# Kernel optimization log

Measured on AMD Instinct MI355X. Metric: run time of the kernel, lower is better.

## Reference

```python
import math
import jax, jax.numpy as jnp
import numpy as np

B, S, D, H = 1, 4096, 1024, 16
HD = D // H


def setup_inputs() -> dict:
    key = jax.random.key(0)
    ks = jax.random.split(key, 11)
    s = 0.02
    inp = {
        "q": jax.random.normal(ks[0], (B, S, D), jnp.float32),
        "k": jax.random.normal(ks[1], (B, S, D), jnp.float32),
        "v": jax.random.normal(ks[2], (B, S, D), jnp.float32),
        # causal boolean mask, broadcastable over [B, H, S, S]
        "mask": jnp.tril(jnp.ones((S, S), jnp.bool_))[None, None],
        "Wq": jax.random.normal(ks[3], (D, D), jnp.float32) * s,
        "bq": jnp.zeros((D,), jnp.float32),
        "Wk": jax.random.normal(ks[4], (D, D), jnp.float32) * s,
        "bk": jnp.zeros((D,), jnp.float32),
        "Wv": jax.random.normal(ks[5], (D, D), jnp.float32) * s,
        "bv": jnp.zeros((D,), jnp.float32),
        "Wo": jax.random.normal(ks[6], (D, D), jnp.float32) * s,
        "bo": jnp.zeros((D,), jnp.float32),
    }
    return inp


def reference(q, k, v, mask, Wq, bq, Wk, bk, Wv, bv, Wo, bo):
    # projections (torch Linear: x @ W.T + b; here W is stored already transposed)
    qp = (q @ Wq + bq).reshape(B, S, H, HD)
    kp = (k @ Wk + bk).reshape(B, S, H, HD)
    vp = (v @ Wv + bv).reshape(B, S, H, HD)
    # scores: [B, H, S, S]
    scores = jnp.einsum("bqhd,bkhd->bhqk", qp, kp) / math.sqrt(HD)
    scores = jnp.where(mask, scores, -jnp.inf)
    attn = jax.nn.softmax(scores, axis=-1)
    # context: [B, H, S, HD] -> [B, S, D]
    ctx = jnp.einsum("bhqk,bkhd->bqhd", attn, vp).reshape(B, S, D)
    return ctx @ Wo + bo
```

## Files before the change

kernel.cpp:

```cpp
#include <hip/hip_runtime.h>
#include <hip/hip_bf16.h>


#define S_LEN 4096
#define D_DIM 1024
#define NHEAD 16
#define HDIM  64

typedef __hip_bfloat16 bf16;
typedef __attribute__((ext_vector_type(8))) short bf16x8v;
typedef __attribute__((ext_vector_type(4))) float f32x4;
typedef __attribute__((ext_vector_type(2))) unsigned int u32x2;

#define MFMA16(a, b, c) __builtin_amdgcn_mfma_f32_16x16x32_bf16((a), (b), (c), 0, 0, 0)

#if __has_builtin(__builtin_amdgcn_exp2f)
#define EXP2F(x) __builtin_amdgcn_exp2f(x)
#else
#define EXP2F(x) exp2f(x)
#endif

#define QSCALE (0.125f * 1.4426950408889634f)

template<int N> struct IC { static constexpr int value = N; };

__device__ __forceinline__ void async_cp16(const void* g, void* l) {
    __builtin_amdgcn_global_load_lds(
        (const __attribute__((address_space(1))) unsigned int*)g,
        (__attribute__((address_space(3))) unsigned int*)l, 16, 0, 0);
}

__device__ __forceinline__ unsigned int cvtpk_bf16(float lo, float hi) {
    unsigned int r;
    asm("v_cvt_pk_bf16_f32 %0, %1, %2" : "=v"(r) : "v"(lo), "v"(hi));
    return r;
}

__global__ __launch_bounds__(256) void cvt_bf16_k(
    const float* __restrict__ x0, const float* __restrict__ x1,
    const float* __restrict__ x2,
    bf16* __restrict__ y0, bf16* __restrict__ y1, bf16* __restrict__ y2)
{
    const float* x = (blockIdx.z == 0) ? x0 : (blockIdx.z == 1) ? x1 : x2;
    bf16*       y = (blockIdx.z == 0) ? y0 : (blockIdx.z == 1) ? y1 : y2;
    const size_t i = ((size_t)blockIdx.x * 256 + threadIdx.x);
    const float4 v = ((const float4*)x)[i];
    union { bf16 h[4]; short4 s; } u;
    u.h[0] = __float2bfloat16(v.x);
    u.h[1] = __float2bfloat16(v.y);
    u.h[2] = __float2bfloat16(v.z);
    u.h[3] = __float2bfloat16(v.w);
    ((short4*)y)[i] = u.s;
}

__global__ __launch_bounds__(256) void transpose_cvt_k(
    const float* __restrict__ W0, const float* __restrict__ W1,
    const float* __restrict__ W2, const float* __restrict__ W3,
    bf16* __restrict__ T0, bf16* __restrict__ T1,
    bf16* __restrict__ T2, bf16* __restrict__ T3)
{
    const float* W = (blockIdx.z == 0) ? W0 : (blockIdx.z == 1) ? W1
                   : (blockIdx.z == 2) ? W2 : W3;
    bf16*       Wt = (blockIdx.z == 0) ? T0 : (blockIdx.z == 1) ? T1
                   : (blockIdx.z == 2) ? T2 : T3;
    __shared__ float t[32][33];
    const int bx = blockIdx.x << 5, by = blockIdx.y << 5;
    const int tx = threadIdx.x & 31, ty = threadIdx.x >> 5;
#pragma unroll
    for (int i = 0; i < 32; i += 8)
        t[ty + i][tx] = W[(size_t)(by + ty + i) * D_DIM + bx + tx];
    __syncthreads();
#pragma unroll
    for (int i = 0; i < 32; i += 8)
        Wt[(size_t)(bx + ty + i) * D_DIM + by + tx] = __float2bfloat16(t[tx][ty + i]);
}

struct GemmJob {
    const bf16* A; const bf16* Wt; const float* bias; void* out;
    int mode; float scale;
};

__global__ __launch_bounds__(256) void gemm_k(GemmJob j0, GemmJob j1, GemmJob j2)
{
    const GemmJob j = (blockIdx.z == 0) ? j0 : (blockIdx.z == 1) ? j1 : j2;
    const int K = D_DIM;

    const int nx  = gridDim.x;
    const int lin = blockIdx.y * nx + blockIdx.x;
    const int per = (nx * gridDim.y) >> 3;
    const int bmn = (lin & 7) * per + (lin >> 3);
    const int bn = (bmn % nx) << 6;
    const int bm = (bmn / nx) << 7;

    const int tid = threadIdx.x;
    const int w = tid >> 6, lane = tid & 63;
    const int col = lane & 15, g = lane >> 4;
    const int wr = (w >> 1) << 6, wc = (w & 1) << 5;

    __shared__ bf16 As[2][128 * 64];
    __shared__ bf16 Bs[2][64 * 64];

    f32x4 acc[4][2];
#pragma unroll
    for (int i = 0; i < 4; ++i)
#pragma unroll
        for (int jj = 0; jj < 2; ++jj) acc[i][jj] = (f32x4){0.f, 0.f, 0.f, 0.f};

    auto stage = [&](int buf, int kb) {
#pragma unroll
        for (int e = 0; e < 4; ++e) {
            const int l2 = (e << 8) + tid;
            const int row = l2 >> 3, kc = l2 & 7;
            async_cp16(j.A + (size_t)(bm + row) * K + kb + (kc << 3), &As[buf][l2 << 3]);
        }
#pragma unroll
        for (int e = 0; e < 2; ++e) {
            const int l2 = (e << 8) + tid;
            const int row = l2 >> 3, kc = l2 & 7;
            async_cp16(j.Wt + (size_t)(bn + row) * K + kb + (kc << 3), &Bs[buf][l2 << 3]);
        }
    };

    stage(0, 0);
    __syncthreads();
    int cur = 0;

    for (int kb = 0; kb < K; kb += 64) {
        if (kb + 64 < K) stage(cur ^ 1, kb + 64);

#pragma unroll
        for (int s = 0; s < 2; ++s) {
            bf16x8v af[4], bfv[2];
#pragma unroll
            for (int i = 0; i < 4; ++i)
                af[i] = *(const bf16x8v*)&As[cur][((wr + (i << 4) + col) << 6) + (s << 5) + (g << 3)];
#pragma unroll
            for (int jj = 0; jj < 2; ++jj)
                bfv[jj] = *(const bf16x8v*)&Bs[cur][((wc + (jj << 4) + col) << 6) + (s << 5) + (g << 3)];
#pragma unroll
            for (int i = 0; i < 4; ++i)
#pragma unroll
                for (int jj = 0; jj < 2; ++jj)
                    acc[i][jj] = MFMA16(af[i], bfv[jj], acc[i][jj]);
        }

        __syncthreads();
        cur ^= 1;
    }

#pragma unroll
    for (int i = 0; i < 4; ++i)
#pragma unroll
    for (int jj = 0; jj < 2; ++jj)
#pragma unroll
    for (int reg = 0; reg < 4; ++reg) {
        const int row = bm + wr + (i << 4) + (g << 2) + reg;
        const int cg  = bn + wc + (jj << 4) + col;
        const float vv = (acc[i][jj][reg] + j.bias[cg]) * j.scale;
        if (j.mode == 0)
            ((bf16*)j.out)[(((size_t)(cg >> 6)) * S_LEN + row) * HDIM + (cg & 63)] =
                __float2bfloat16(vv);
        else if (j.mode == 2)
            ((bf16*)j.out)[((size_t)(cg >> 6) * HDIM + (cg & 63)) * S_LEN + row] =
                __float2bfloat16(vv);
        else
            ((float*)j.out)[(size_t)row * D_DIM + cg] = vv;
    }
}

__global__ __launch_bounds__(256) void attn_mfma_k(
    const bf16* __restrict__ Qp, const bf16* __restrict__ Kp,
    const bf16* __restrict__ Vt, bf16* __restrict__ ctx,
    float* __restrict__ Opart, float* __restrict__ lpart, int mode)
{
    __shared__ bf16 Ks[2][4096];
    __shared__ bf16 Vs[2][4096];

    const int bid = blockIdx.x;
    const int h   = bid & 15;
    const int jid = bid >> 4;

    int qb, t0, nt, chunk;
    bool dosplit, hdiag;
    if (mode == 1) {
        if (jid < 16)      { qb = 31 - jid;        t0 = 2*qb - 30; nt = 32;        dosplit = true;  chunk = 1; hdiag = true;  }
        else if (jid < 32) { qb = 31 - (jid - 16); t0 = 0;         nt = 2*qb - 30; dosplit = true;  chunk = 0; hdiag = false; }
        else               { qb = 15 - (jid - 32); t0 = 0;         nt = 2*qb + 2;  dosplit = false; chunk = 0; hdiag = true;  }
    } else {
        qb = 31 - jid; t0 = 0; nt = 2*qb + 2; dosplit = false; chunk = 0; hdiag = true;
    }

    const int q0  = qb << 7;
    const int tid = threadIdx.x, w = tid >> 6, lane = tid & 63;
    const int col = lane & 15, g = lane >> 4;

    const bf16* Kh = Kp + (size_t)h * S_LEN * HDIM;
    const bf16* Vh = Vt + (size_t)h * HDIM * S_LEN;

    const int qrowA = q0 + (w << 4) + col;
    const int qrowB = qrowA + 64;
    const size_t qbaseA = ((size_t)h * S_LEN + qrowA) * HDIM + (g << 3);
    const size_t qbaseB = qbaseA + (size_t)64 * HDIM;
    const bf16x8v qfA0 = *(const bf16x8v*)(Qp + qbaseA);
    const bf16x8v qfA1 = *(const bf16x8v*)(Qp + qbaseA + 32);
    const bf16x8v qfB0 = *(const bf16x8v*)(Qp + qbaseB);
    const bf16x8v qfB1 = *(const bf16x8v*)(Qp + qbaseB + 32);

    float plA = 0.f, plB = 0.f;
    f32x4 accA[4], accB[4];
#pragma unroll
    for (int t = 0; t < 4; ++t) {
        accA[t] = (f32x4){0.f, 0.f, 0.f, 0.f};
        accB[t] = (f32x4){0.f, 0.f, 0.f, 0.f};
    }

    auto stage = [&](int buf, int kb) {
        const int kk0 = kb << 6;
#pragma unroll
        for (int e = 0; e < 2; ++e) {
            const int lin = (e << 8) + tid;
            const int t = lin >> 7, G = (lin >> 4) & 7, c = lin & 15;
            async_cp16(Kh + (size_t)(kk0 + (t << 4) + c) * HDIM + (G << 3),
                       &Ks[buf][lin << 3]);
            async_cp16(Vh + (size_t)((t << 4) + c) * S_LEN + kk0 + (G << 3),
                       &Vs[buf][lin << 3]);
        }
    };

    auto body = [&](auto mtag, int kb, int cur) {
        constexpr int MODE = decltype(mtag)::value;
        const int kk0 = kb << 6;
        const bf16* Kc = Ks[cur];
        const bf16* Vc = Vs[cur];

        f32x4 saA[4], saB[4];
#pragma unroll
        for (int t = 0; t < 4; ++t) {
            saA[t] = (f32x4){0.f, 0.f, 0.f, 0.f};
            saB[t] = (f32x4){0.f, 0.f, 0.f, 0.f};
        }
        __builtin_amdgcn_s_setprio(1);
#pragma unroll
        for (int t = 0; t < 4; ++t) {
            const bf16x8v kf0 = *(const bf16x8v*)&Kc[((t << 7) + (g << 4) + col) << 3];
            const bf16x8v kf1 = *(const bf16x8v*)&Kc[((t << 7) + 64 + (g << 4) + col) << 3];
            if (MODE != 2) {
                saA[t] = MFMA16(kf0, qfA0, saA[t]);
                saA[t] = MFMA16(kf1, qfA1, saA[t]);
            }
            saB[t] = MFMA16(kf0, qfB0, saB[t]);
            saB[t] = MFMA16(kf1, qfB1, saB[t]);
        }
        __builtin_amdgcn_s_setprio(0);

#pragma unroll
        for (int t = 0; t < 4; ++t) {
#pragma unroll
            for (int reg = 0; reg < 4; ++reg) {
                const int kidx = kk0 + (t << 4) + (g << 2) + reg;
                if (MODE != 2) {
                    float pA;
                    if (MODE == 1 && kidx > qrowA) pA = 0.f;
                    else                           pA = EXP2F(saA[t][reg]);
                    plA += pA; saA[t][reg] = pA;
                }
                float pB;
                if (MODE == 2 && kidx > qrowB) pB = 0.f;
                else                           pB = EXP2F(saB[t][reg]);
                plB += pB; saB[t][reg] = pB;
            }
        }

        union { unsigned int wd[4]; bf16x8v v; } pA0, pA1, pB0, pB1;
        if (MODE != 2) {
            unsigned int c0[4], c1[4];
#pragma unroll
            for (int t = 0; t < 4; ++t) {
                c0[t] = cvtpk_bf16(saA[t][0], saA[t][1]);
                c1[t] = cvtpk_bf16(saA[t][2], saA[t][3]);
            }
            u32x2 r0 = __builtin_amdgcn_permlane32_swap(c0[0], c0[1], false, false);
            u32x2 r1 = __builtin_amdgcn_permlane32_swap(c1[0], c1[1], false, false);
            u32x2 s0 = __builtin_amdgcn_permlane16_swap(r0[0], r0[1], false, false);
            u32x2 s1 = __builtin_amdgcn_permlane16_swap(r1[0], r1[1], false, false);
            pA0.wd[0] = s0[0]; pA0.wd[1] = s1[0]; pA0.wd[2] = s0[1]; pA0.wd[3] = s1[1];
            r0 = __builtin_amdgcn_permlane32_swap(c0[2], c0[3], false, false);
            r1 = __builtin_amdgcn_permlane32_swap(c1[2], c1[3], false, false);
            s0 = __builtin_amdgcn_permlane16_swap(r0[0], r0[1], false, false);
            s1 = __builtin_amdgcn_permlane16_swap(r1[0], r1[1], false, false);
            pA1.wd[0] = s0[0]; pA1.wd[1] = s1[0]; pA1.wd[2] = s0[1]; pA1.wd[3] = s1[1];
        }
        {
            unsigned int c0[4], c1[4];
#pragma unroll
            for (int t = 0; t < 4; ++t) {
                c0[t] = cvtpk_bf16(saB[t][0], saB[t][1]);
                c1[t] = cvtpk_bf16(saB[t][2], saB[t][3]);
            }
            u32x2 r0 = __builtin_amdgcn_permlane32_swap(c0[0], c0[1], false, false);
            u32x2 r1 = __builtin_amdgcn_permlane32_swap(c1[0], c1[1], false, false);
            u32x2 s0 = __builtin_amdgcn_permlane16_swap(r0[0], r0[1], false, false);
            u32x2 s1 = __builtin_amdgcn_permlane16_swap(r1[0], r1[1], false, false);
            pB0.wd[0] = s0[0]; pB0.wd[1] = s1[0]; pB0.wd[2] = s0[1]; pB0.wd[3] = s1[1];
            r0 = __builtin_amdgcn_permlane32_swap(c0[2], c0[3], false, false);
            r1 = __builtin_amdgcn_permlane32_swap(c1[2], c1[3], false, false);
            s0 = __builtin_amdgcn_permlane16_swap(r0[0], r0[1], false, false);
            s1 = __builtin_amdgcn_permlane16_swap(r1[0], r1[1], false, false);
            pB1.wd[0] = s0[0]; pB1.wd[1] = s1[0]; pB1.wd[2] = s0[1]; pB1.wd[3] = s1[1];
        }

        __builtin_amdgcn_s_setprio(1);
#pragma unroll
        for (int t = 0; t < 4; ++t) {
            const bf16x8v vf0 = *(const bf16x8v*)&Vc[((t << 7) + (g << 4) + col) << 3];
            const bf16x8v vf1 = *(const bf16x8v*)&Vc[((t << 7) + 64 + (g << 4) + col) << 3];
            if (MODE != 2) {
                accA[t] = MFMA16(vf0, pA0.v, accA[t]);
                accA[t] = MFMA16(vf1, pA1.v, accA[t]);
            }
            accB[t] = MFMA16(vf0, pB0.v, accB[t]);
            accB[t] = MFMA16(vf1, pB1.v, accB[t]);
        }
        __builtin_amdgcn_s_setprio(0);
    };

    int kb = t0, cur = 0;
    const int kend = t0 + nt;
    stage(0, kb);
    __syncthreads();

    const int nmain = hdiag ? nt - 2 : nt;
    for (int i = 0; i < nmain; ++i, ++kb) {
        if (kb + 1 < kend) stage(cur ^ 1, kb + 1);
        body(IC<0>{}, kb, cur);
        __syncthreads();
        cur ^= 1;
    }
    if (hdiag) {
        stage(cur ^ 1, kb + 1);
        body(IC<1>{}, kb, cur);
        __syncthreads();
        cur ^= 1; ++kb;
        body(IC<2>{}, kb, cur);
    }

    float lA = plA, lB = plB;
    lA += __shfl_xor(lA, 16); lA += __shfl_xor(lA, 32);
    lB += __shfl_xor(lB, 16); lB += __shfl_xor(lB, 32);

    if (!dosplit) {
        const float invA = 1.f / lA;
        const float invB = 1.f / lB;
#pragma unroll
        for (int t = 0; t < 4; ++t) {
            union { bf16 hh[4]; short4 s4; } uA, uB;
#pragma unroll
            for (int reg = 0; reg < 4; ++reg) {
                uA.hh[reg] = __float2bfloat16(accA[t][reg] * invA);
                uB.hh[reg] = __float2bfloat16(accB[t][reg] * invB);
            }
            *(short4*)&ctx[(size_t)qrowA * D_DIM + h * HDIM + (t << 4) + (g << 2)] = uA.s4;
            *(short4*)&ctx[(size_t)qrowB * D_DIM + h * HDIM + (t << 4) + (g << 2)] = uB.s4;
        }
    } else {
        const int srowA = ((qb - 16) << 7) + (w << 4) + col;
        const int srowB = srowA + 64;
        float* OpA = Opart + (((size_t)chunk * NHEAD + h) * 2048 + srowA) * HDIM;
        float* OpB = Opart + (((size_t)chunk * NHEAD + h) * 2048 + srowB) * HDIM;
#pragma unroll
        for (int t = 0; t < 4; ++t) {
            *(f32x4*)&OpA[(t << 4) + (g << 2)] = accA[t];
            *(f32x4*)&OpB[(t << 4) + (g << 2)] = accB[t];
        }
        if (g == 0) {
            lpart[((size_t)chunk * NHEAD + h) * 2048 + srowA] = lA;
            lpart[((size_t)chunk * NHEAD + h) * 2048 + srowB] = lB;
        }
    }
}

__global__ __launch_bounds__(256) void combine_k(
    const float* __restrict__ Opart, const float* __restrict__ lpart,
    bf16* __restrict__ ctx)
{
    const int tid = threadIdx.x;
    const int row = (blockIdx.x << 4) + (tid >> 4);
    const int d4  = (tid & 15) << 2;
    const int h   = row >> 11;
    const int srow = row & 2047;
    const float4 a = *(const float4*)&Opart[(size_t)row * HDIM + d4];
    const float4 b = *(const float4*)&Opart[(size_t)(32768 + row) * HDIM + d4];
    const float inv = 1.f / (lpart[row] + lpart[32768 + row]);
    union { bf16 hh[4]; short4 s4; } u;
    u.hh[0] = __float2bfloat16((a.x + b.x) * inv);
    u.hh[1] = __float2bfloat16((a.y + b.y) * inv);
    u.hh[2] = __float2bfloat16((a.z + b.z) * inv);
    u.hh[3] = __float2bfloat16((a.w + b.w) * inv);
    const int qrow = 2048 + srow;
    *(short4*)&ctx[(size_t)qrow * D_DIM + h * HDIM + d4] = u.s4;
}

extern "C" void kernel_launch(void* const* d_in, const int* in_sizes, int n_in,
                              void* d_out, int out_size, void* d_ws, size_t ws_size,
                              hipStream_t stream)
{
    const float* q  = (const float*)d_in[0];
    const float* k  = (const float*)d_in[1];
    const float* v  = (const float*)d_in[2];
    const float* Wq = (const float*)d_in[4];
    const float* bq = (const float*)d_in[5];
    const float* Wk = (const float*)d_in[6];
    const float* bk = (const float*)d_in[7];
    const float* Wv = (const float*)d_in[8];
    const float* bv = (const float*)d_in[9];
    const float* Wo = (const float*)d_in[10];
    const float* bo = (const float*)d_in[11];

    const size_t PE  = (size_t)S_LEN * D_DIM;
    const size_t WTE = (size_t)D_DIM * D_DIM;

    const dim3 tg(32, 32, 4);
    const dim3 gg(D_DIM / 64, S_LEN / 128, 1);
    const dim3 gg3(D_DIM / 64, S_LEN / 128, 3);
    const dim3 cg((unsigned)(PE / 1024), 1, 3);

    if (ws_size >= (size_t)64 * 1024 * 1024) {
        bf16* Qb = (bf16*)d_ws;
        bf16* Kb = Qb + PE;
        bf16* Vb = Kb + PE;
        bf16* Qp = Vb + PE;
        bf16* Kp = Qp + PE;
        bf16* Vt = Kp + PE;
        bf16* Wtq = Vt + PE;
        bf16* Wtk = Wtq + WTE;
        bf16* Wtv = Wtk + WTE;
        bf16* Wto = Wtv + WTE;
        bf16* ctx = Qb;
        float* Opart = (float*)Kb;
        float* lpart = (float*)(Wto + WTE);

        transpose_cvt_k<<<tg, 256, 0, stream>>>(Wq, Wk, Wv, Wo, Wtq, Wtk, Wtv, Wto);
        cvt_bf16_k<<<cg, 256, 0, stream>>>(q, k, v, Qb, Kb, Vb);

        GemmJob jq{Qb, Wtq, bq, Qp, 0, QSCALE};
        GemmJob jk{Kb, Wtk, bk, Kp, 0, 1.0f};
        GemmJob jv{Vb, Wtv, bv, Vt, 2, 1.0f};
        gemm_k<<<gg3, 256, 0, stream>>>(jq, jk, jv);

        attn_mfma_k<<<dim3(768), 256, 0, stream>>>(Qp, Kp, Vt, ctx, Opart, lpart, 1);
        combine_k<<<dim3(2048), 256, 0, stream>>>(Opart, lpart, ctx);

        GemmJob jo{ctx, Wto, bo, d_out, 1, 1.0f};
        gemm_k<<<gg, 256, 0, stream>>>(jo, jo, jo);
    } else {
        bf16* X  = (bf16*)d_ws;
        bf16* Qp = X + PE;
        bf16* Kp = Qp + PE;
        bf16* Vt = Kp + PE;
        bf16* Wtq = Vt + PE;
        bf16* Wtk = Wtq + WTE;
        bf16* Wtv = Wtk + WTE;
        bf16* Wto = Wtv + WTE;

        transpose_cvt_k<<<tg, 256, 0, stream>>>(Wq, Wk, Wv, Wo, Wtq, Wtk, Wtv, Wto);

        const dim3 cg1((unsigned)(PE / 1024), 1, 1);
        cvt_bf16_k<<<cg1, 256, 0, stream>>>(q, q, q, X, X, X);
        GemmJob jq{X, Wtq, bq, Qp, 0, QSCALE};
        gemm_k<<<gg, 256, 0, stream>>>(jq, jq, jq);
        cvt_bf16_k<<<cg1, 256, 0, stream>>>(k, k, k, X, X, X);
        GemmJob jk{X, Wtk, bk, Kp, 0, 1.0f};
        gemm_k<<<gg, 256, 0, stream>>>(jk, jk, jk);
        cvt_bf16_k<<<cg1, 256, 0, stream>>>(v, v, v, X, X, X);
        GemmJob jv{X, Wtv, bv, Vt, 2, 1.0f};
        gemm_k<<<gg, 256, 0, stream>>>(jv, jv, jv);

        attn_mfma_k<<<dim3(512), 256, 0, stream>>>(Qp, Kp, Vt, X, nullptr, nullptr, 0);

        GemmJob jo{X, Wto, bo, d_out, 1, 1.0f};
        gemm_k<<<gg, 256, 0, stream>>>(jo, jo, jo);
    }
}
```

Before: 307.3 us.

## Use persistent atomic work queue for attention and XOR-swizzle GEMM shared memory

The attention kernel becomes persistent: 512 blocks pull jobs from a global atomic counter, ordered so the longest causal tiles go first. This is meant to improve load balance across the 768 variable-length jobs. The counter is reset inside the weight-transpose kernel. Separately, the GEMM shared-memory tiles are XOR-swizzled by row to cut LDS bank conflicts on the MFMA fragment loads. Risks are extra __syncthreads and atomic overhead per job, plus reliance on the counter reset running before attention.

```diff
diff --git a/kernel.cpp b/kernel.cpp
--- a/kernel.cpp
+++ b/kernel.cpp
@@ -57,8 +57,12 @@
     const float* __restrict__ W0, const float* __restrict__ W1,
     const float* __restrict__ W2, const float* __restrict__ W3,
     bf16* __restrict__ T0, bf16* __restrict__ T1,
-    bf16* __restrict__ T2, bf16* __restrict__ T3)
+    bf16* __restrict__ T2, bf16* __restrict__ T3,
+    int* jq)
 {
+    if (jq && blockIdx.x == 0 && blockIdx.y == 0 && blockIdx.z == 0 &&
+        threadIdx.x == 0)
+        *jq = 0;
     const float* W = (blockIdx.z == 0) ? W0 : (blockIdx.z == 1) ? W1
                    : (blockIdx.z == 2) ? W2 : W3;
     bf16*       Wt = (blockIdx.z == 0) ? T0 : (blockIdx.z == 1) ? T1
@@ -96,6 +100,7 @@
     const int w = tid >> 6, lane = tid & 63;
     const int col = lane & 15, g = lane >> 4;
     const int wr = (w >> 1) << 6, wc = (w & 1) << 5;
+    const int c7 = col & 7;
 
     __shared__ bf16 As[2][128 * 64];
     __shared__ bf16 Bs[2][64 * 64];
@@ -111,13 +116,15 @@
         for (int e = 0; e < 4; ++e) {
             const int l2 = (e << 8) + tid;
             const int row = l2 >> 3, kc = l2 & 7;
-            async_cp16(j.A + (size_t)(bm + row) * K + kb + (kc << 3), &As[buf][l2 << 3]);
+            async_cp16(j.A + (size_t)(bm + row) * K + kb + ((kc ^ (row & 7)) << 3),
+                       &As[buf][l2 << 3]);
         }
 #pragma unroll
         for (int e = 0; e < 2; ++e) {
             const int l2 = (e << 8) + tid;
             const int row = l2 >> 3, kc = l2 & 7;
-            async_cp16(j.Wt + (size_t)(bn + row) * K + kb + (kc << 3), &Bs[buf][l2 << 3]);
+            async_cp16(j.Wt + (size_t)(bn + row) * K + kb + ((kc ^ (row & 7)) << 3),
+                       &Bs[buf][l2 << 3]);
         }
     };
 
@@ -130,13 +137,14 @@
 
 #pragma unroll
         for (int s = 0; s < 2; ++s) {
+            const int gsw = (((s << 2) + g) ^ c7) << 3;
             bf16x8v af[4], bfv[2];
 #pragma unroll
             for (int i = 0; i < 4; ++i)
-                af[i] = *(const bf16x8v*)&As[cur][((wr + (i << 4) + col) << 6) + (s << 5) + (g << 3)];
+                af[i] = *(const bf16x8v*)&As[cur][((wr + (i << 4) + col) << 6) + gsw];
 #pragma unroll
             for (int jj = 0; jj < 2; ++jj)
-                bfv[jj] = *(const bf16x8v*)&Bs[cur][((wc + (jj << 4) + col) << 6) + (s << 5) + (g << 3)];
+                bfv[jj] = *(const bf16x8v*)&Bs[cur][((wc + (jj << 4) + col) << 6) + gsw];
 #pragma unroll
             for (int i = 0; i < 4; ++i)
 #pragma unroll
@@ -171,211 +179,226 @@
 __global__ __launch_bounds__(256) void attn_mfma_k(
     const bf16* __restrict__ Qp, const bf16* __restrict__ Kp,
     const bf16* __restrict__ Vt, bf16* __restrict__ ctx,
-    float* __restrict__ Opart, float* __restrict__ lpart, int mode)
+    float* __restrict__ Opart, float* __restrict__ lpart,
+    int* __restrict__ jq, int mode)
 {
     __shared__ bf16 Ks[2][4096];
     __shared__ bf16 Vs[2][4096];
-
-    const int bid = blockIdx.x;
-    const int h   = bid & 15;
-    const int jid = bid >> 4;
-
-    int qb, t0, nt, chunk;
-    bool dosplit, hdiag;
-    if (mode == 1) {
-        if (jid < 16)      { qb = 31 - jid;        t0 = 2*qb - 30; nt = 32;        dosplit = true;  chunk = 1; hdiag = true;  }
-        else if (jid < 32) { qb = 31 - (jid - 16); t0 = 0;         nt = 2*qb - 30; dosplit = true;  chunk = 0; hdiag = false; }
-        else               { qb = 15 - (jid - 32); t0 = 0;         nt = 2*qb + 2;  dosplit = false; chunk = 0; hdiag = true;  }
-    } else {
-        qb = 31 - jid; t0 = 0; nt = 2*qb + 2; dosplit = false; chunk = 0; hdiag = true;
-    }
-
-    const int q0  = qb << 7;
+    __shared__ int jbox;
+
     const int tid = threadIdx.x, w = tid >> 6, lane = tid & 63;
     const int col = lane & 15, g = lane >> 4;
 
-    const bf16* Kh = Kp + (size_t)h * S_LEN * HDIM;
-    const bf16* Vh = Vt + (size_t)h * HDIM * S_LEN;
-
-    const int qrowA = q0 + (w << 4) + col;
-    const int qrowB = qrowA + 64;
-    const size_t qbaseA = ((size_t)h * S_LEN + qrowA) * HDIM + (g << 3);
-    const size_t qbaseB = qbaseA + (size_t)64 * HDIM;
-    const bf16x8v qfA0 = *(const bf16x8v*)(Qp + qbaseA);
-    const bf16x8v qfA1 = *(const bf16x8v*)(Qp + qbaseA + 32);
-    const bf16x8v qfB0 = *(const bf16x8v*)(Qp + qbaseB);
-    const bf16x8v qfB1 = *(const bf16x8v*)(Qp + qbaseB + 32);
-
-    float plA = 0.f, plB = 0.f;
-    f32x4 accA[4], accB[4];
-#pragma unroll
-    for (int t = 0; t < 4; ++t) {
-        accA[t] = (f32x4){0.f, 0.f, 0.f, 0.f};
-        accB[t] = (f32x4){0.f, 0.f, 0.f, 0.f};
-    }
-
-    auto stage = [&](int buf, int kb) {
-        const int kk0 = kb << 6;
-#pragma unroll
-        for (int e = 0; e < 2; ++e) {
-            const int lin = (e << 8) + tid;
-            const int t = lin >> 7, G = (lin >> 4) & 7, c = lin & 15;
-            async_cp16(Kh + (size_t)(kk0 + (t << 4) + c) * HDIM + (G << 3),
-                       &Ks[buf][lin << 3]);
-            async_cp16(Vh + (size_t)((t << 4) + c) * S_LEN + kk0 + (G << 3),
-                       &Vs[buf][lin << 3]);
-        }
-    };
-
-    auto body = [&](auto mtag, int kb, int cur) {
-        constexpr int MODE = decltype(mtag)::value;
-        const int kk0 = kb << 6;
-        const bf16* Kc = Ks[cur];
-        const bf16* Vc = Vs[cur];
-
-        f32x4 saA[4], saB[4];
+    for (;;) {
+        int h, qb, t0, nt, chunk;
+        bool dosplit, hdiag;
+        if (mode == 1) {
+            if (tid == 0) jbox = atomicAdd(jq, 1);
+            __syncthreads();
+            const int jjob = jbox;
+            if (jjob >= 768) return;
+            if (jjob < 256) {
+                h = jjob & 15; qb = 16 + (jjob >> 4);
+                t0 = 2 * qb - 30; nt = 32; dosplit = true; chunk = 1; hdiag = true;
+            } else {
+                const int jj = jjob - 256;
+                const int s = jj >> 5, r = (jj >> 4) & 1;
+                h = jj & 15;
+                if (r == 0) { qb = 31 - s; t0 = 0; nt = 2 * qb - 30; dosplit = true;  chunk = 0; hdiag = false; }
+                else        { qb = 15 - s; t0 = 0; nt = 2 * qb + 2;  dosplit = false; chunk = 0; hdiag = true;  }
+            }
+        } else {
+            const int bid = blockIdx.x;
+            h = bid & 15; qb = 31 - (bid >> 4);
+            t0 = 0; nt = 2 * qb + 2; dosplit = false; chunk = 0; hdiag = true;
+        }
+
+        const int q0 = qb << 7;
+        const bf16* Kh = Kp + (size_t)h * S_LEN * HDIM;
+        const bf16* Vh = Vt + (size_t)h * HDIM * S_LEN;
+
+        const int qrowA = q0 + (w << 4) + col;
+        const int qrowB = qrowA + 64;
+        const size_t qbaseA = ((size_t)h * S_LEN + qrowA) * HDIM + (g << 3);
+        const size_t qbaseB = qbaseA + (size_t)64 * HDIM;
+        const bf16x8v qfA0 = *(const bf16x8v*)(Qp + qbaseA);
+        const bf16x8v qfA1 = *(const bf16x8v*)(Qp + qbaseA + 32);
+        const bf16x8v qfB0 = *(const bf16x8v*)(Qp + qbaseB);
+        const bf16x8v qfB1 = *(const bf16x8v*)(Qp + qbaseB + 32);
+
+        float plA = 0.f, plB = 0.f;
+        f32x4 accA[4], accB[4];
 #pragma unroll
         for (int t = 0; t < 4; ++t) {
-            saA[t] = (f32x4){0.f, 0.f, 0.f, 0.f};
-            saB[t] = (f32x4){0.f, 0.f, 0.f, 0.f};
-        }
-        __builtin_amdgcn_s_setprio(1);
-#pragma unroll
-        for (int t = 0; t < 4; ++t) {
-            const bf16x8v kf0 = *(const bf16x8v*)&Kc[((t << 7) + (g << 4) + col) << 3];
-            const bf16x8v kf1 = *(const bf16x8v*)&Kc[((t << 7) + 64 + (g << 4) + col) << 3];
+            accA[t] = (f32x4){0.f, 0.f, 0.f, 0.f};
+            accB[t] = (f32x4){0.f, 0.f, 0.f, 0.f};
+        }
+
+        auto stage = [&](int buf, int kb) {
+            const int kk0 = kb << 6;
+#pragma unroll
+            for (int e = 0; e < 2; ++e) {
+                const int lin = (e << 8) + tid;
+                const int t = lin >> 7, G = (lin >> 4) & 7, c = lin & 15;
+                async_cp16(Kh + (size_t)(kk0 + (t << 4) + c) * HDIM + (G << 3),
+                           &Ks[buf][lin << 3]);
+                async_cp16(Vh + (size_t)((t << 4) + c) * S_LEN + kk0 + (G << 3),
+                           &Vs[buf][lin << 3]);
+            }
+        };
+
+        auto body = [&](auto mtag, int kb, int cur) {
+            constexpr int MODE = decltype(mtag)::value;
+            const int kk0 = kb << 6;
+            const bf16* Kc = Ks[cur];
+            const bf16* Vc = Vs[cur];
+
+            f32x4 saA[4], saB[4];
+#pragma unroll
+            for (int t = 0; t < 4; ++t) {
+                saA[t] = (f32x4){0.f, 0.f, 0.f, 0.f};
+                saB[t] = (f32x4){0.f, 0.f, 0.f, 0.f};
+            }
+            __builtin_amdgcn_s_setprio(1);
+#pragma unroll
+            for (int t = 0; t < 4; ++t) {
+                const bf16x8v kf0 = *(const bf16x8v*)&Kc[((t << 7) + (g << 4) + col) << 3];
+                const bf16x8v kf1 = *(const bf16x8v*)&Kc[((t << 7) + 64 + (g << 4) + col) << 3];
+                if (MODE != 2) {
+                    saA[t] = MFMA16(kf0, qfA0, saA[t]);
+                    saA[t] = MFMA16(kf1, qfA1, saA[t]);
+                }
+                saB[t] = MFMA16(kf0, qfB0, saB[t]);
+                saB[t] = MFMA16(kf1, qfB1, saB[t]);
+            }
+            __builtin_amdgcn_s_setprio(0);
+
+#pragma unroll
+            for (int t = 0; t < 4; ++t) {
+#pragma unroll
+                for (int reg = 0; reg < 4; ++reg) {
+                    const int kidx = kk0 + (t << 4) + (g << 2) + reg;
+                    if (MODE != 2) {
+                        float pA;
+                        if (MODE == 1 && kidx > qrowA) pA = 0.f;
+                        else                           pA = EXP2F(saA[t][reg]);
+                        plA += pA; saA[t][reg] = pA;
+                    }
+                    float pB;
+                    if (MODE == 2 && kidx > qrowB) pB = 0.f;
+                    else                           pB = EXP2F(saB[t][reg]);
+                    plB += pB; saB[t][reg] = pB;
+                }
+            }
+
+            union { unsigned int wd[4]; bf16x8v v; } pA0, pA1, pB0, pB1;
             if (MODE != 2) {
-                saA[t] = MFMA16(kf0, qfA0, saA[t]);
-                saA[t] = MFMA16(kf1, qfA1, saA[t]);
-            }
-            saB[t] = MFMA16(kf0, qfB0, saB[t]);
-            saB[t] = MFMA16(kf1, qfB1, saB[t]);
-        }
-        __builtin_amdgcn_s_setprio(0);
-
-#pragma unroll
-        for (int t = 0; t < 4; ++t) {
-#pragma unroll
-            for (int reg = 0; reg < 4; ++reg) {
-                const int kidx = kk0 + (t << 4) + (g << 2) + reg;
+                unsigned int c0[4], c1[4];
+#pragma unroll
+                for (int t = 0; t < 4; ++t) {
+                    c0[t] = cvtpk_bf16(saA[t][0], saA[t][1]);
+                    c1[t] = cvtpk_bf16(saA[t][2], saA[t][3]);
+                }
+                u32x2 r0 = __builtin_amdgcn_permlane32_swap(c0[0], c0[1], false, false);
+                u32x2 r1 = __builtin_amdgcn_permlane32_swap(c1[0], c1[1], false, false);
+                u32x2 s0 = __builtin_amdgcn_permlane16_swap(r0[0], r0[1], false, false);
+                u32x2 s1 = __builtin_amdgcn_permlane16_swap(r1[0], r1[1], false, false);
+                pA0.wd[0] = s0[0]; pA0.wd[1] = s1[0]; pA0.wd[2] = s0[1]; pA0.wd[3] = s1[1];
+                r0 = __builtin_amdgcn_permlane32_swap(c0[2], c0[3], false, false);
+                r1 = __builtin_amdgcn_permlane32_swap(c1[2], c1[3], false, false);
+                s0 = __builtin_amdgcn_permlane16_swap(r0[0], r0[1], false, false);
+                s1 = __builtin_amdgcn_permlane16_swap(r1[0], r1[1], false, false);
+                pA1.wd[0] = s0[0]; pA1.wd[1] = s1[0]; pA1.wd[2] = s0[1]; pA1.wd[3] = s1[1];
+            }
+            {
+                unsigned int c0[4], c1[4];
+#pragma unroll
+                for (int t = 0; t < 4; ++t) {
+                    c0[t] = cvtpk_bf16(saB[t][0], saB[t][1]);
+                    c1[t] = cvtpk_bf16(saB[t][2], saB[t][3]);
+                }
+                u32x2 r0 = __builtin_amdgcn_permlane32_swap(c0[0], c0[1], false, false);
+                u32x2 r1 = __builtin_amdgcn_permlane32_swap(c1[0], c1[1], false, false);
+                u32x2 s0 = __builtin_amdgcn_permlane16_swap(r0[0], r0[1], false, false);
+                u32x2 s1 = __builtin_amdgcn_permlane16_swap(r1[0], r1[1], false, false);
+                pB0.wd[0] = s0[0]; pB0.wd[1] = s1[0]; pB0.wd[2] = s0[1]; pB0.wd[3] = s1[1];
+                r0 = __builtin_amdgcn_permlane32_swap(c0[2], c0[3], false, false);
+                r1 = __builtin_amdgcn_permlane32_swap(c1[2], c1[3], false, false);
+                s0 = __builtin_amdgcn_permlane16_swap(r0[0], r0[1], false, false);
+                s1 = __builtin_amdgcn_permlane16_swap(r1[0], r1[1], false, false);
+                pB1.wd[0] = s0[0]; pB1.wd[1] = s1[0]; pB1.wd[2] = s0[1]; pB1.wd[3] = s1[1];
+            }
+
+            __builtin_amdgcn_s_setprio(1);
+#pragma unroll
+            for (int t = 0; t < 4; ++t) {
+                const bf16x8v vf0 = *(const bf16x8v*)&Vc[((t << 7) + (g << 4) + col) << 3];
+                const bf16x8v vf1 = *(const bf16x8v*)&Vc[((t << 7) + 64 + (g << 4) + col) << 3];
                 if (MODE != 2) {
-                    float pA;
-                    if (MODE == 1 && kidx > qrowA) pA = 0.f;
-                    else                           pA = EXP2F(saA[t][reg]);
-                    plA += pA; saA[t][reg] = pA;
+                    accA[t] = MFMA16(vf0, pA0.v, accA[t]);
+                    accA[t] = MFMA16(vf1, pA1.v, accA[t]);
                 }
-                float pB;
-                if (MODE == 2 && kidx > qrowB) pB = 0.f;
-                else                           pB = EXP2F(saB[t][reg]);
-                plB += pB; saB[t][reg] = pB;
-            }
-        }
-
-        union { unsigned int wd[4]; bf16x8v v; } pA0, pA1, pB0, pB1;
-        if (MODE != 2) {
-            unsigned int c0[4], c1[4];
+                accB[t] = MFMA16(vf0, pB0.v, accB[t]);
+                accB[t] = MFMA16(vf1, pB1.v, accB[t]);
+            }
+            __builtin_amdgcn_s_setprio(0);
+        };
+
+        int kb = t0, cur = 0;
+        const int kend = t0 + nt;
+        stage(0, kb);
+        __syncthreads();
+
+        const int nmain = hdiag ? nt - 2 : nt;
+        for (int i = 0; i < nmain; ++i, ++kb) {
+            if (kb + 1 < kend) stage(cur ^ 1, kb + 1);
+            body(IC<0>{}, kb, cur);
+            __syncthreads();
+            cur ^= 1;
+        }
+        if (hdiag) {
+            stage(cur ^ 1, kb + 1);
+            body(IC<1>{}, kb, cur);
+            __syncthreads();
+            cur ^= 1; ++kb;
+            body(IC<2>{}, kb, cur);
+        }
+
+        float lA = plA, lB = plB;
+        lA += __shfl_xor(lA, 16); lA += __shfl_xor(lA, 32);
+        lB += __shfl_xor(lB, 16); lB += __shfl_xor(lB, 32);
+
+        if (!dosplit) {
+            const float invA = 1.f / lA;
+            const float invB = 1.f / lB;
 #pragma unroll
             for (int t = 0; t < 4; ++t) {
-                c0[t] = cvtpk_bf16(saA[t][0], saA[t][1]);
-                c1[t] = cvtpk_bf16(saA[t][2], saA[t][3]);
-            }
-            u32x2 r0 = __builtin_amdgcn_permlane32_swap(c0[0], c0[1], false, false);
-            u32x2 r1 = __builtin_amdgcn_permlane32_swap(c1[0], c1[1], false, false);
-            u32x2 s0 = __builtin_amdgcn_permlane16_swap(r0[0], r0[1], false, false);
-            u32x2 s1 = __builtin_amdgcn_permlane16_swap(r1[0], r1[1], false, false);
-            pA0.wd[0] = s0[0]; pA0.wd[1] = s1[0]; pA0.wd[2] = s0[1]; pA0.wd[3] = s1[1];
-            r0 = __builtin_amdgcn_permlane32_swap(c0[2], c0[3], false, false);
-            r1 = __builtin_amdgcn_permlane32_swap(c1[2], c1[3], false, false);
-            s0 = __builtin_amdgcn_permlane16_swap(r0[0], r0[1], false, false);
-            s1 = __builtin_amdgcn_permlane16_swap(r1[0], r1[1], false, false);
-            pA1.wd[0] = s0[0]; pA1.wd[1] = s1[0]; pA1.wd[2] = s0[1]; pA1.wd[3] = s1[1];
-        }
-        {
-            unsigned int c0[4], c1[4];
+                union { bf16 hh[4]; short4 s4; } uA, uB;
+#pragma unroll
+                for (int reg = 0; reg < 4; ++reg) {
+                    uA.hh[reg] = __float2bfloat16(accA[t][reg] * invA);
+                    uB.hh[reg] = __float2bfloat16(accB[t][reg] * invB);
+                }
+                *(short4*)&ctx[(size_t)qrowA * D_DIM + h * HDIM + (t << 4) + (g << 2)] = uA.s4;
+                *(short4*)&ctx[(size_t)qrowB * D_DIM + h * HDIM + (t << 4) + (g << 2)] = uB.s4;
+            }
+        } else {
+            const int srowA = ((qb - 16) << 7) + (w << 4) + col;
+            const int srowB = srowA + 64;
+            float* OpA = Opart + (((size_t)chunk * NHEAD + h) * 2048 + srowA) * HDIM;
+            float* OpB = Opart + (((size_t)chunk * NHEAD + h) * 2048 + srowB) * HDIM;
 #pragma unroll
             for (int t = 0; t < 4; ++t) {
-                c0[t] = cvtpk_bf16(saB[t][0], saB[t][1]);
-                c1[t] = cvtpk_bf16(saB[t][2], saB[t][3]);
-            }
-            u32x2 r0 = __builtin_amdgcn_permlane32_swap(c0[0], c0[1], false, false);
-            u32x2 r1 = __builtin_amdgcn_permlane32_swap(c1[0], c1[1], false, false);
-            u32x2 s0 = __builtin_amdgcn_permlane16_swap(r0[0], r0[1], false, false);
-            u32x2 s1 = __builtin_amdgcn_permlane16_swap(r1[0], r1[1], false, false);
-            pB0.wd[0] = s0[0]; pB0.wd[1] = s1[0]; pB0.wd[2] = s0[1]; pB0.wd[3] = s1[1];
-            r0 = __builtin_amdgcn_permlane32_swap(c0[2], c0[3], false, false);
-            r1 = __builtin_amdgcn_permlane32_swap(c1[2], c1[3], false, false);
-            s0 = __builtin_amdgcn_permlane16_swap(r0[0], r0[1], false, false);
-            s1 = __builtin_amdgcn_permlane16_swap(r1[0], r1[1], false, false);
-            pB1.wd[0] = s0[0]; pB1.wd[1] = s1[0]; pB1.wd[2] = s0[1]; pB1.wd[3] = s1[1];
-        }
-
-        __builtin_amdgcn_s_setprio(1);
-#pragma unroll
-        for (int t = 0; t < 4; ++t) {
-            const bf16x8v vf0 = *(const bf16x8v*)&Vc[((t << 7) + (g << 4) + col) << 3];
-            const bf16x8v vf1 = *(const bf16x8v*)&Vc[((t << 7) + 64 + (g << 4) + col) << 3];
-            if (MODE != 2) {
-                accA[t] = MFMA16(vf0, pA0.v, accA[t]);
-                accA[t] = MFMA16(vf1, pA1.v, accA[t]);
-            }
-            accB[t] = MFMA16(vf0, pB0.v, accB[t]);
-            accB[t] = MFMA16(vf1, pB1.v, accB[t]);
-        }
-        __builtin_amdgcn_s_setprio(0);
-    };
-
-    int kb = t0, cur = 0;
-    const int kend = t0 + nt;
-    stage(0, kb);
-    __syncthreads();
-
-    const int nmain = hdiag ? nt - 2 : nt;
-    for (int i = 0; i < nmain; ++i, ++kb) {
-        if (kb + 1 < kend) stage(cur ^ 1, kb + 1);
-        body(IC<0>{}, kb, cur);
-        __syncthreads();
-        cur ^= 1;
-    }
-    if (hdiag) {
-        stage(cur ^ 1, kb + 1);
-        body(IC<1>{}, kb, cur);
-        __syncthreads();
-        cur ^= 1; ++kb;
-        body(IC<2>{}, kb, cur);
-    }
-
-    float lA = plA, lB = plB;
-    lA += __shfl_xor(lA, 16); lA += __shfl_xor(lA, 32);
-    lB += __shfl_xor(lB, 16); lB += __shfl_xor(lB, 32);
-
-    if (!dosplit) {
-        const float invA = 1.f / lA;
-        const float invB = 1.f / lB;
-#pragma unroll
-        for (int t = 0; t < 4; ++t) {
-            union { bf16 hh[4]; short4 s4; } uA, uB;
-#pragma unroll
-            for (int reg = 0; reg < 4; ++reg) {
-                uA.hh[reg] = __float2bfloat16(accA[t][reg] * invA);
-                uB.hh[reg] = __float2bfloat16(accB[t][reg] * invB);
-            }
-            *(short4*)&ctx[(size_t)qrowA * D_DIM + h * HDIM + (t << 4) + (g << 2)] = uA.s4;
-            *(short4*)&ctx[(size_t)qrowB * D_DIM + h * HDIM + (t << 4) + (g << 2)] = uB.s4;
-        }
-    } else {
-        const int srowA = ((qb - 16) << 7) + (w << 4) + col;
-        const int srowB = srowA + 64;
-        float* OpA = Opart + (((size_t)chunk * NHEAD + h) * 2048 + srowA) * HDIM;
-        float* OpB = Opart + (((size_t)chunk * NHEAD + h) * 2048 + srowB) * HDIM;
-#pragma unroll
-        for (int t = 0; t < 4; ++t) {
-            *(f32x4*)&OpA[(t << 4) + (g << 2)] = accA[t];
-            *(f32x4*)&OpB[(t << 4) + (g << 2)] = accB[t];
-        }
-        if (g == 0) {
-            lpart[((size_t)chunk * NHEAD + h) * 2048 + srowA] = lA;
-            lpart[((size_t)chunk * NHEAD + h) * 2048 + srowB] = lB;
-        }
+                *(f32x4*)&OpA[(t << 4) + (g << 2)] = accA[t];
+                *(f32x4*)&OpB[(t << 4) + (g << 2)] = accB[t];
+            }
+            if (g == 0) {
+                lpart[((size_t)chunk * NHEAD + h) * 2048 + srowA] = lA;
+                lpart[((size_t)chunk * NHEAD + h) * 2048 + srowB] = lB;
+            }
+        }
+
+        if (mode != 1) return;
     }
 }
 
@@ -438,20 +461,21 @@
         bf16* ctx = Qb;
         float* Opart = (float*)Kb;
         float* lpart = (float*)(Wto + WTE);
-
-        transpose_cvt_k<<<tg, 256, 0, stream>>>(Wq, Wk, Wv, Wo, Wtq, Wtk, Wtv, Wto);
+        int*   jq    = (int*)(lpart + 2 * NHEAD * 2048);
+
+        transpose_cvt_k<<<tg, 256, 0, stream>>>(Wq, Wk, Wv, Wo, Wtq, Wtk, Wtv, Wto, jq);
         cvt_bf16_k<<<cg, 256, 0, stream>>>(q, k, v, Qb, Kb, Vb);
 
-        GemmJob jq{Qb, Wtq, bq, Qp, 0, QSCALE};
-        GemmJob jk{Kb, Wtk, bk, Kp, 0, 1.0f};
-        GemmJob jv{Vb, Wtv, bv, Vt, 2, 1.0f};
-        gemm_k<<<gg3, 256, 0, stream>>>(jq, jk, jv);
-
-        attn_mfma_k<<<dim3(768), 256, 0, stream>>>(Qp, Kp, Vt, ctx, Opart, lpart, 1);
+        GemmJob jqj{Qb, Wtq, bq, Qp, 0, QSCALE};
+        GemmJob jkj{Kb, Wtk, bk, Kp, 0, 1.0f};
+        GemmJob jvj{Vb, Wtv, bv, Vt, 2, 1.0f};
+        gemm_k<<<gg3, 256, 0, stream>>>(jqj, jkj, jvj);
+
+        attn_mfma_k<<<dim3(512), 256, 0, stream>>>(Qp, Kp, Vt, ctx, Opart, lpart, jq, 1);
         combine_k<<<dim3(2048), 256, 0, stream>>>(Opart, lpart, ctx);
 
-        GemmJob jo{ctx, Wto, bo, d_out, 1, 1.0f};
-        gemm_k<<<gg, 256, 0, stream>>>(jo, jo, jo);
+        GemmJob joj{ctx, Wto, bo, d_out, 1, 1.0f};
+        gemm_k<<<gg, 256, 0, stream>>>(joj, joj, joj);
     } else {
         bf16* X  = (bf16*)d_ws;
         bf16* Qp = X + PE;
@@ -462,22 +486,22 @@
         bf16* Wtv = Wtk + WTE;
         bf16* Wto = Wtv + WTE;
 
-        transpose_cvt_k<<<tg, 256, 0, stream>>>(Wq, Wk, Wv, Wo, Wtq, Wtk, Wtv, Wto);
+        transpose_cvt_k<<<tg, 256, 0, stream>>>(Wq, Wk, Wv, Wo, Wtq, Wtk, Wtv, Wto, nullptr);
 
         const dim3 cg1((unsigned)(PE / 1024), 1, 1);
         cvt_bf16_k<<<cg1, 256, 0, stream>>>(q, q, q, X, X, X);
-        GemmJob jq{X, Wtq, bq, Qp, 0, QSCALE};
-        gemm_k<<<gg, 256, 0, stream>>>(jq, jq, jq);
+        GemmJob jqj{X, Wtq, bq, Qp, 0, QSCALE};
+        gemm_k<<<gg, 256, 0, stream>>>(jqj, jqj, jqj);
         cvt_bf16_k<<<cg1, 256, 0, stream>>>(k, k, k, X, X, X);
-        GemmJob jk{X, Wtk, bk, Kp, 0, 1.0f};
-        gemm_k<<<gg, 256, 0, stream>>>(jk, jk, jk);
+        GemmJob jkj{X, Wtk, bk, Kp, 0, 1.0f};
+        gemm_k<<<gg, 256, 0, stream>>>(jkj, jkj, jkj);
         cvt_bf16_k<<<cg1, 256, 0, stream>>>(v, v, v, X, X, X);
-        GemmJob jv{X, Wtv, bv, Vt, 2, 1.0f};
-        gemm_k<<<gg, 256, 0, stream>>>(jv, jv, jv);
-
-        attn_mfma_k<<<dim3(512), 256, 0, stream>>>(Qp, Kp, Vt, X, nullptr, nullptr, 0);
-
-        GemmJob jo{X, Wto, bo, d_out, 1, 1.0f};
-        gemm_k<<<gg, 256, 0, stream>>>(jo, jo, jo);
+        GemmJob jvj{X, Wtv, bv, Vt, 2, 1.0f};
+        gemm_k<<<gg, 256, 0, stream>>>(jvj, jvj, jvj);
+
+        attn_mfma_k<<<dim3(512), 256, 0, stream>>>(Qp, Kp, Vt, X, nullptr, nullptr, nullptr, 0);
+
+        GemmJob joj{X, Wto, bo, d_out, 1, 1.0f};
+        gemm_k<<<gg, 256, 0, stream>>>(joj, joj, joj);
     }
 }
```

After: 298.1 us. -3.0%, faster.
